# Optimization experiments

Hardware: AMD Instinct MI355X
Metric: run time of the kernel (lower is better)

The kernel has to match this reference:

```python
import jax, jax.numpy as jnp
import numpy as np

V, P, T = 30522, 1024, 2
D, H, F, L = 768, 12, 3072, 4
HD = D // H
EPS = 1e-12


def layer_norm(x, g, b):
    mu = jnp.mean(x, axis=-1, keepdims=True)
    var = jnp.mean((x - mu) ** 2, axis=-1, keepdims=True)
    return (x - mu) * jax.lax.rsqrt(var + EPS) * g + b


def setup_inputs() -> dict:
    key = jax.random.key(0)
    ks = iter(jax.random.split(key, 32))
    s = 0.02
    inp = {
        "x": jax.random.randint(next(ks), (4, 1024), 0, V, dtype=jnp.int32),
        "word_emb": jax.random.normal(next(ks), (V, D), jnp.float32) * s,
        "pos_emb": jax.random.normal(next(ks), (P, D), jnp.float32) * s,
        "type_emb": jax.random.normal(next(ks), (T, D), jnp.float32) * s,
        "emb_g": jnp.ones((D,), jnp.float32),
        "emb_b": jnp.zeros((D,), jnp.float32),
        "Wq": jax.random.normal(next(ks), (L, D, D), jnp.float32) * s,
        "bq": jnp.zeros((L, D), jnp.float32),
        "Wk": jax.random.normal(next(ks), (L, D, D), jnp.float32) * s,
        "bk": jnp.zeros((L, D), jnp.float32),
        "Wv": jax.random.normal(next(ks), (L, D, D), jnp.float32) * s,
        "bv": jnp.zeros((L, D), jnp.float32),
        "Wo": jax.random.normal(next(ks), (L, D, D), jnp.float32) * s,
        "bo": jnp.zeros((L, D), jnp.float32),
        "ln1_g": jnp.ones((L, D), jnp.float32),
        "ln1_b": jnp.zeros((L, D), jnp.float32),
        "W1": jax.random.normal(next(ks), (L, D, F), jnp.float32) * s,
        "b1": jnp.zeros((L, F), jnp.float32),
        "W2": jax.random.normal(next(ks), (L, F, D), jnp.float32) * s,
        "b2": jnp.zeros((L, D), jnp.float32),
        "ln2_g": jnp.ones((L, D), jnp.float32),
        "ln2_b": jnp.zeros((L, D), jnp.float32),
        "Wp": jax.random.normal(next(ks), (D, D), jnp.float32) * s,
        "bp": jnp.zeros((D,), jnp.float32),
    }
    return inp


def _bert_forward(x, word_emb, pos_emb, type_emb, emb_g, emb_b,
                  Wq, bq, Wk, bk, Wv, bv, Wo, bo, ln1_g, ln1_b,
                  W1, b1, W2, b2, ln2_g, ln2_b, Wp, bp):
    B, S = x.shape
    # Embeddings (token_type_ids are all zeros in the original forward)
    h = word_emb[x] + pos_emb[:S][None, :, :] + type_emb[0][None, None, :]
    h = layer_norm(h, emb_g, emb_b)

    scale = 1.0 / np.sqrt(HD).astype(np.float32)

    def step(h, p):
        (wq, bq_, wk, bk_, wv, bv_, wo, bo_, g1, b1_, w1, bi1, w2, bi2, g2, b2_) = p
        q = (h @ wq + bq_).reshape(B, S, H, HD)
        k = (h @ wk + bk_).reshape(B, S, H, HD)
        v = (h @ wv + bv_).reshape(B, S, H, HD)
        att = jnp.einsum("bqhd,bkhd->bhqk", q, k) * scale
        att = jax.nn.softmax(att, axis=-1)
        o = jnp.einsum("bhqk,bkhd->bqhd", att, v).reshape(B, S, D)
        # attention output: dense + residual + LN
        h = layer_norm(o @ wo + bo_ + h, g1, b1_)
        # FFN (note: original applies GELU twice and has NO residual here)
        inter = jax.nn.gelu(h @ w1 + bi1, approximate=False)
        h = layer_norm(jax.nn.gelu(inter @ w2 + bi2, approximate=False), g2, b2_)
        return h, None

    params = (Wq, bq, Wk, bk, Wv, bv, Wo, bo, ln1_g, ln1_b, W1, b1, W2, b2, ln2_g, ln2_b)
    h, _ = jax.lax.scan(step, h, params)
    # Pooler on final hidden states (loop in original overwrites output each iter)
    return jnp.tanh(h[:, 0] @ Wp + bp)


def reference(x, word_emb, pos_emb, type_emb, emb_g, emb_b,
              Wq, bq, Wk, bk, Wv, bv, Wo, bo, ln1_g, ln1_b,
              W1, b1, W2, b2, ln2_g, ln2_b, Wp, bp):
    return _bert_forward(x, word_emb, pos_emb, type_emb, emb_g, emb_b,
                         Wq, bq, Wk, bk, Wv, bv, Wo, bo, ln1_g, ln1_b,
                         W1, b1, W2, b2, ln2_g, ln2_b, Wp, bp)
```

## Files before the change

kernel.cpp:

```cpp
#include <hip/hip_runtime.h>
#include <math.h>

namespace {

constexpr int B  = 4;
constexpr int S  = 1024;
constexpr int D  = 768;
constexpr int H  = 12;
constexpr int HD = 64;
constexpr int F  = 3072;
constexpr int L  = 4;
constexpr int M  = B * S;
constexpr int NQKV = 3 * D;
constexpr int NQK = 2 * D;

typedef __attribute__((ext_vector_type(4))) float    f32x4;
typedef _Float16 f16x8 __attribute__((ext_vector_type(8)));
typedef __attribute__((ext_vector_type(8))) unsigned short u16x8;
typedef __attribute__((ext_vector_type(4))) unsigned short u16x4;

__device__ __forceinline__ unsigned short f2h_u(float f) {
    _Float16 h = (_Float16)f;
    return __builtin_bit_cast(unsigned short, h);
}
__device__ __forceinline__ float h2f(unsigned short u) {
    return (float)__builtin_bit_cast(_Float16, u);
}

__device__ __forceinline__ void gload16(const void* gptr, void* ldsptr) {
    __builtin_amdgcn_global_load_lds(
        (const __attribute__((address_space(1))) unsigned int*)gptr,
        (__attribute__((address_space(3))) unsigned int*)ldsptr,
        16, 0, 0);
}

__device__ __forceinline__ float wave_sum(float v) {
#pragma unroll
    for (int off = 32; off; off >>= 1) v += __shfl_xor(v, off, 64);
    return v;
}
__device__ __forceinline__ float block_sum256(float v, float* sm) {
    v = wave_sum(v);
    __syncthreads();
    if ((threadIdx.x & 63) == 0) sm[threadIdx.x >> 6] = v;
    __syncthreads();
    return sm[0] + sm[1] + sm[2] + sm[3];
}

__device__ __forceinline__ void transpose_tile(const float* __restrict__ src,
                                               unsigned short* __restrict__ dst,
                                               int R, int C) {
    __shared__ float tile[32][33];
    const int cb = blockIdx.x * 32, rb = blockIdx.y * 32;
    const int t = threadIdx.x;
    {
        const int r = t >> 3, cq = (t & 7) * 4;
        const float4 v = *(const float4*)&src[(size_t)(rb + r) * C + cb + cq];
        tile[r][cq + 0] = v.x; tile[r][cq + 1] = v.y;
        tile[r][cq + 2] = v.z; tile[r][cq + 3] = v.w;
    }
    __syncthreads();
    {
        const int dc = t >> 3, rq = (t & 7) * 4;
        u16x4 o;
#pragma unroll
        for (int j = 0; j < 4; ++j) o[j] = f2h_u(tile[rq + j][dc]);
        *(u16x4*)&dst[(size_t)(cb + dc) * R + rb + rq] = o;
    }
}

__global__ __launch_bounds__(256) void transpose_qkvo_kernel(
    const float* __restrict__ Wq, const float* __restrict__ Wk,
    const float* __restrict__ Wv, const float* __restrict__ Wo,
    unsigned short* __restrict__ Wqkv_t, unsigned short* __restrict__ Wo_t) {
    const int z = blockIdx.z;
    const int l = z >> 2, which = z & 3;
    const float* src = (which == 0 ? Wq : which == 1 ? Wk : which == 2 ? Wv : Wo)
                       + (size_t)l * D * D;
    unsigned short* dst = (which < 3)
        ? Wqkv_t + ((size_t)l * NQKV + which * D) * D
        : Wo_t + (size_t)l * D * D;
    transpose_tile(src, dst, D, D);
}

__global__ __launch_bounds__(256) void transpose_w_kernel(
    const float* __restrict__ src0, unsigned short* __restrict__ dst0, int R, int C) {
    const int l = blockIdx.z;
    transpose_tile(src0 + (size_t)l * R * C, dst0 + (size_t)l * R * C, R, C);
}

__global__ __launch_bounds__(256) void bias_concat_kernel(
    const float* __restrict__ bq, const float* __restrict__ bk,
    const float* __restrict__ bv, float* __restrict__ bqkv) {
    const int i = blockIdx.x * 256 + threadIdx.x;
    if (i >= L * NQKV) return;
    const int l = i / NQKV, j = i % NQKV;
    float v = (j < D) ? bq[l * D + j] : (j < 2 * D) ? bk[l * D + j - D] : bv[l * D + j - 2 * D];
    bqkv[i] = v;
}

__global__ __launch_bounds__(256) void embed_ln_kernel(
    const int* __restrict__ x, const float* __restrict__ we,
    const float* __restrict__ pe, const float* __restrict__ te,
    const float* __restrict__ g, const float* __restrict__ bb,
    float* __restrict__ hres, unsigned short* __restrict__ hh) {
    __shared__ float sm[4];
    const int row = blockIdx.x;
    const int s = row & (S - 1);
    const int tok = x[row];
    const int t = threadIdx.x;
    const bool act = t < 192;
    const int d = t * 4;
    float v[4] = {};
    if (act) {
        const float4 w = *(const float4*)&we[(size_t)tok * D + d];
        const float4 p = *(const float4*)&pe[(size_t)s * D + d];
        const float4 tt = *(const float4*)&te[d];
        v[0] = w.x + p.x + tt.x; v[1] = w.y + p.y + tt.y;
        v[2] = w.z + p.z + tt.z; v[3] = w.w + p.w + tt.w;
    }
    const float mu = block_sum256(v[0] + v[1] + v[2] + v[3], sm) * (1.0f / D);
    float lvar = 0.f;
    if (act) {
#pragma unroll
        for (int i = 0; i < 4; ++i) { float dv = v[i] - mu; lvar += dv * dv; }
    }
    const float var = block_sum256(lvar, sm) * (1.0f / D);
    const float inv = rsqrtf(var + 1e-12f);
    if (act) {
        const float4 g4 = *(const float4*)&g[d];
        const float4 b4 = *(const float4*)&bb[d];
        float o[4];
        o[0] = (v[0] - mu) * inv * g4.x + b4.x;
        o[1] = (v[1] - mu) * inv * g4.y + b4.y;
        o[2] = (v[2] - mu) * inv * g4.z + b4.z;
        o[3] = (v[3] - mu) * inv * g4.w + b4.w;
        *(float4*)&hres[(size_t)row * D + d] = make_float4(o[0], o[1], o[2], o[3]);
        u16x4 ob;
#pragma unroll
        for (int i = 0; i < 4; ++i) ob[i] = f2h_u(o[i]);
        *(u16x4*)&hh[(size_t)row * D + d] = ob;
    }
}

template <int NP, bool GELU_, bool HAS_RES>
__global__ __launch_bounds__(256) void ln_reduce_kernel(
    const unsigned short* __restrict__ parts,
    const float* __restrict__ bias,
    const float* __restrict__ res,
    const float* __restrict__ g, const float* __restrict__ bb,
    float* __restrict__ outres, unsigned short* __restrict__ outh) {
    __shared__ float sm[4];
    const int row = blockIdx.x;
    const int t = threadIdx.x;
    const bool act = t < 192;
    const int d = t * 4;
    float v[4] = {};
    if (act) {
        const float4 bi = *(const float4*)&bias[d];
        v[0] = bi.x; v[1] = bi.y; v[2] = bi.z; v[3] = bi.w;
#pragma unroll
        for (int pp = 0; pp < NP; ++pp) {
            const u16x4 pu = *(const u16x4*)&parts[(size_t)pp * M * D + (size_t)row * D + d];
#pragma unroll
            for (int i = 0; i < 4; ++i) v[i] += h2f(pu[i]);
        }
        if (HAS_RES) {
            const float4 rv = *(const float4*)&res[(size_t)row * D + d];
            v[0] += rv.x; v[1] += rv.y; v[2] += rv.z; v[3] += rv.w;
        }
        if (GELU_) {
#pragma unroll
            for (int i = 0; i < 4; ++i)
                v[i] = 0.5f * v[i] * (1.0f + erff(v[i] * 0.70710678118654752f));
        }
    }
    const float mu = block_sum256(v[0] + v[1] + v[2] + v[3], sm) * (1.0f / D);
    float lvar = 0.f;
    if (act) {
#pragma unroll
        for (int i = 0; i < 4; ++i) { float dv = v[i] - mu; lvar += dv * dv; }
    }
    const float var = block_sum256(lvar, sm) * (1.0f / D);
    const float inv = rsqrtf(var + 1e-12f);
    if (act) {
        const float4 g4 = *(const float4*)&g[d];
        const float4 b4 = *(const float4*)&bb[d];
        float o[4];
        o[0] = (v[0] - mu) * inv * g4.x + b4.x;
        o[1] = (v[1] - mu) * inv * g4.y + b4.y;
        o[2] = (v[2] - mu) * inv * g4.z + b4.z;
        o[3] = (v[3] - mu) * inv * g4.w + b4.w;
        *(float4*)&outres[(size_t)row * D + d] = make_float4(o[0], o[1], o[2], o[3]);
        u16x4 ob;
#pragma unroll
        for (int i = 0; i < 4; ++i) ob[i] = f2h_u(o[i]);
        *(u16x4*)&outh[(size_t)row * D + d] = ob;
    }
}

#define GEMM_STAGE(buf, k0)                                                          \
    do {                                                                             \
        gload16(Ab + (size_t)(rowBase + r0) * LDA + (k0) + c0 * 8, &Asl[buf][ldsOff0]); \
        gload16(Ab + (size_t)(rowBase + r1) * LDA + (k0) + c1 * 8, &Asl[buf][ldsOff1]); \
        gload16(Bb + (size_t)(colBase + r0) * LDA + (k0) + c0 * 8, &Bsl[buf][ldsOff0]); \
        gload16(Bb + (size_t)(colBase + r1) * LDA + (k0) + c1 * 8, &Bsl[buf][ldsOff1]); \
    } while (0)

#define GEMM_BODY(A_, Bw_, LDA_, KLEN_)                                              \
    constexpr int BK = 32;                                                           \
    __shared__ unsigned short Asl[3][128 * BK];                                      \
    __shared__ unsigned short Bsl[3][128 * BK];                                      \
    const unsigned short* Ab = (A_);                                                 \
    const unsigned short* Bb = (Bw_);                                                \
    const int LDA = (LDA_);                                                          \
    const int t = threadIdx.x;                                                       \
    const int lane = t & 63;                                                         \
    const int wid = t >> 6;                                                          \
    const int lr = lane & 15;                                                        \
    const int kh = lane >> 4;                                                        \
    const int wrBase = (wid >> 1) * 64;                                              \
    const int wcBase = (wid & 1) * 64;                                               \
    const int rowBase = blockIdx.y * 128;                                            \
    const int colBase = blockIdx.x * 128;                                            \
    f32x4 acc[4][4] = {};                                                            \
    const int r0 = t >> 2, c0 = (t & 3) ^ ((r0 >> 1) & 3);                           \
    const int s_hi = 256 + t;                                                        \
    const int r1 = s_hi >> 2, c1 = (s_hi & 3) ^ ((r1 >> 1) & 3);                     \
    const unsigned ldsOff0 = (unsigned)((t & 192) * 8);                              \
    const unsigned ldsOff1 = (unsigned)((256 + (t & 192)) * 8);                      \
    const int nt = (KLEN_) / BK;                                                     \
    GEMM_STAGE(0, 0);                                                                \
    GEMM_STAGE(1, BK);                                                               \
    int p = 0;                                                                       \
    for (int tt = 0; tt < nt; ++tt) {                                                \
        if (tt + 1 < nt) asm volatile("s_waitcnt vmcnt(4)" ::: "memory");            \
        else             asm volatile("s_waitcnt vmcnt(0)" ::: "memory");            \
        __builtin_amdgcn_s_barrier();                                                \
        __builtin_amdgcn_sched_barrier(0);                                           \
        if (tt + 2 < nt) {                                                           \
            int nb = p + 2; if (nb >= 3) nb -= 3;                                    \
            GEMM_STAGE(nb, (tt + 2) * BK);                                           \
        }                                                                            \
        f16x8 af[4], bfr[4];                                                         \
        _Pragma("unroll")                                                            \
        for (int mi = 0; mi < 4; ++mi) {                                             \
            const int ar = wrBase + mi * 16 + lr;                                    \
            const int ch = kh ^ ((ar >> 1) & 3);                                     \
            af[mi] = *(const f16x8*)&Asl[p][ar * BK + ch * 8];                       \
        }                                                                            \
        _Pragma("unroll")                                                            \
        for (int nj = 0; nj < 4; ++nj) {                                             \
            const int bc = wcBase + nj * 16 + lr;                                    \
            const int ch = kh ^ ((bc >> 1) & 3);                                     \
            bfr[nj] = *(const f16x8*)&Bsl[p][bc * BK + ch * 8];                      \
        }                                                                            \
        _Pragma("unroll")                                                            \
        for (int mi = 0; mi < 4; ++mi)                                               \
            _Pragma("unroll")                                                        \
            for (int nj = 0; nj < 4; ++nj)                                           \
                acc[mi][nj] = __builtin_amdgcn_mfma_f32_16x16x32_f16(                \
                    af[mi], bfr[nj], acc[mi][nj], 0, 0, 0);                          \
        p = (p == 2) ? 0 : p + 1;                                                    \
    }

template <int EPI, typename CT>
__global__ __launch_bounds__(256) void gemm_mfma_kernel(
    const unsigned short* __restrict__ A, const unsigned short* __restrict__ Bw,
    const float* __restrict__ bias, CT* __restrict__ C, int N, int K) {
    GEMM_BODY(A, Bw, K, K)
#pragma unroll
    for (int nj = 0; nj < 4; ++nj) {
        const int col = colBase + wcBase + nj * 16 + lr;
        const float bc = bias[col];
#pragma unroll
        for (int mi = 0; mi < 4; ++mi) {
            const int row = rowBase + wrBase + mi * 16 + kh * 4;
#pragma unroll
            for (int j = 0; j < 4; ++j) {
                float v = acc[mi][nj][j] + bc;
                if (EPI == 1) v = 0.5f * v * (1.0f + erff(v * 0.70710678118654752f));
                if constexpr (sizeof(CT) == 4) C[(size_t)(row + j) * N + col] = v;
                else                           C[(size_t)(row + j) * N + col] = f2h_u(v);
            }
        }
    }
}

__global__ __launch_bounds__(256) void gemm_splitk_kernel(
    const unsigned short* __restrict__ A, const unsigned short* __restrict__ Bw,
    unsigned short* __restrict__ Cpart, int N, int Kfull, int Kc) {
    const int z = blockIdx.z;
    GEMM_BODY(A + (size_t)z * Kc, Bw + (size_t)z * Kc, Kfull, Kc)
    unsigned short* Cp = Cpart + (size_t)z * M * N;
#pragma unroll
    for (int nj = 0; nj < 4; ++nj) {
        const int col = colBase + wcBase + nj * 16 + lr;
#pragma unroll
        for (int mi = 0; mi < 4; ++mi) {
            const int row = rowBase + wrBase + mi * 16 + kh * 4;
#pragma unroll
            for (int j = 0; j < 4; ++j)
                Cp[(size_t)(row + j) * N + col] = f2h_u(acc[mi][nj][j]);
        }
    }
}

__global__ __launch_bounds__(256) void gemm_qkv_kernel(
    const unsigned short* __restrict__ A, const unsigned short* __restrict__ Bw,
    const float* __restrict__ bias, unsigned short* __restrict__ qkout,
    unsigned short* __restrict__ vtout) {
    GEMM_BODY(A, Bw, D, D)
    const bool isV = (colBase >= NQK);
#pragma unroll
    for (int nj = 0; nj < 4; ++nj) {
        const int col = colBase + wcBase + nj * 16 + lr;
        const float bc = bias[col];
        if (!isV) {
#pragma unroll
            for (int mi = 0; mi < 4; ++mi) {
                const int row = rowBase + wrBase + mi * 16 + kh * 4;
#pragma unroll
                for (int j = 0; j < 4; ++j)
                    qkout[(size_t)(row + j) * NQK + col] = f2h_u(acc[mi][nj][j] + bc);
            }
        } else {
            const int dd = col - NQK;
            const int h2 = dd >> 6, d6 = dd & 63;
#pragma unroll
            for (int mi = 0; mi < 4; ++mi) {
                const int row = rowBase + wrBase + mi * 16 + kh * 4;
                const int b2 = row >> 10, s2 = row & 1023;
                u16x4 ov;
#pragma unroll
                for (int j = 0; j < 4; ++j) ov[j] = f2h_u(acc[mi][nj][j] + bc);
                *(u16x4*)&vtout[(((size_t)(b2 * H + h2)) * 64 + d6) * S + s2] = ov;
            }
        }
    }
}

__global__ __launch_bounds__(256) void attention_kernel(
    const unsigned short* __restrict__ qk,
    const unsigned short* __restrict__ vt,
    unsigned short* __restrict__ o) {
    __shared__ unsigned short Qs[64 * 64];
    __shared__ unsigned short Ks[2][64 * 64];
    __shared__ unsigned short Vt[2][64 * 64];
    __shared__ _Float16 Ps[4][16 * 64];

    const int t = threadIdx.x;
    const int qt = blockIdx.x;
    const int bh = blockIdx.y;
    const int b = bh / H, hh = bh % H;
    const int w = t >> 6;
    const int lr = t & 15;
    const int kh = (t >> 4) & 3;

    const int r0 = t >> 3;
    const int g0 = (t & 7) ^ (r0 & 7);
    const unsigned lo0 = (unsigned)((t & 192) * 8);
    const unsigned lo1 = (unsigned)(2048 + (t & 192) * 8);

    const unsigned short* kgb = qk + D + hh * HD;
    const unsigned short* vgb = vt + (size_t)bh * 64 * S;

    {
        const size_t qrow0 = (size_t)(b * S + qt * 64);
        gload16(qk + (qrow0 + r0) * NQK + hh * HD + g0 * 8, &Qs[lo0]);
        gload16(qk + (qrow0 + r0 + 32) * NQK + hh * HD + g0 * 8, &Qs[lo1]);
        gload16(kgb + (size_t)(b * S + r0) * NQK + g0 * 8, &Ks[0][lo0]);
        gload16(kgb + (size_t)(b * S + r0 + 32) * NQK + g0 * 8, &Ks[0][lo1]);
        gload16(vgb + (size_t)r0 * S + g0 * 8, &Vt[0][lo0]);
        gload16(vgb + (size_t)(r0 + 32) * S + g0 * 8, &Vt[0][lo1]);
    }
    __syncthreads();

    float m_[4] = {-INFINITY, -INFINITY, -INFINITY, -INFINITY};
    float l_[4] = {};
    f32x4 oacc[4] = {};
    const int swlo = (kh)     ^ (lr & 7);
    const int swhi = (kh + 4) ^ (lr & 7);
    constexpr int NT = S / 64;

    for (int it = 0; it < NT; ++it) {
        const int cur = it & 1;
        if (it + 1 < NT) {
            const int kt = (it + 1) * 64;
            gload16(kgb + (size_t)(b * S + kt + r0) * NQK + g0 * 8, &Ks[cur ^ 1][lo0]);
            gload16(kgb + (size_t)(b * S + kt + r0 + 32) * NQK + g0 * 8, &Ks[cur ^ 1][lo1]);
            gload16(vgb + (size_t)r0 * S + kt + g0 * 8, &Vt[cur ^ 1][lo0]);
            gload16(vgb + (size_t)(r0 + 32) * S + kt + g0 * 8, &Vt[cur ^ 1][lo1]);
        }

        const int qr = w * 16 + lr;
        f16x8 aq0 = *(const f16x8*)&Qs[qr * 64 + swlo * 8];
        f16x8 aq1 = *(const f16x8*)&Qs[qr * 64 + swhi * 8];
        f32x4 sc[4];
        __builtin_amdgcn_s_setprio(1);
#pragma unroll
        for (int nj = 0; nj < 4; ++nj) {
            const int kr = nj * 16 + lr;
            f16x8 b0 = *(const f16x8*)&Ks[cur][kr * 64 + swlo * 8];
            f16x8 b1 = *(const f16x8*)&Ks[cur][kr * 64 + swhi * 8];
            f32x4 z = {};
            z = __builtin_amdgcn_mfma_f32_16x16x32_f16(aq0, b0, z, 0, 0, 0);
            z = __builtin_amdgcn_mfma_f32_16x16x32_f16(aq1, b1, z, 0, 0, 0);
            sc[nj] = z;
        }
        __builtin_amdgcn_s_setprio(0);

        float alpha[4];
#pragma unroll
        for (int j = 0; j < 4; ++j) {
            float rm = fmaxf(fmaxf(sc[0][j], sc[1][j]), fmaxf(sc[2][j], sc[3][j])) * 0.125f;
#pragma unroll
            for (int off = 1; off < 16; off <<= 1) rm = fmaxf(rm, __shfl_xor(rm, off, 64));
            const float mn = fmaxf(m_[j], rm);
            alpha[j] = __expf(m_[j] - mn);
            m_[j] = mn;
        }
        float ph[4][4];
        float rs[4] = {};
#pragma unroll
        for (int nj = 0; nj < 4; ++nj)
#pragma unroll
            for (int j = 0; j < 4; ++j) {
                float p2 = __expf(fmaf(sc[nj][j], 0.125f, -m_[j]));
                ph[nj][j] = p2;
                rs[j] += p2;
            }
#pragma unroll
        for (int j = 0; j < 4; ++j) {
#pragma unroll
            for (int off = 1; off < 16; off <<= 1) rs[j] += __shfl_xor(rs[j], off, 64);
            l_[j] = l_[j] * alpha[j] + rs[j];
        }
        _Float16* psw = &Ps[w][0];
#pragma unroll
        for (int nj = 0; nj < 4; ++nj)
#pragma unroll
            for (int j = 0; j < 4; ++j) {
                const int pr = kh * 4 + j;
                const int pc = nj * 16 + lr;
                psw[pr * 64 + (((pc >> 3) ^ (pr & 7)) * 8) + (pc & 7)] = (_Float16)ph[nj][j];
            }
#pragma unroll
        for (int nj = 0; nj < 4; ++nj)
#pragma unroll
            for (int j = 0; j < 4; ++j) oacc[nj][j] *= alpha[j];

        f16x8 pa0 = *(const f16x8*)&psw[lr * 64 + swlo * 8];
        f16x8 pa1 = *(const f16x8*)&psw[lr * 64 + swhi * 8];
        __builtin_amdgcn_s_setprio(1);
#pragma unroll
        for (int nj = 0; nj < 4; ++nj) {
            const int vr = nj * 16 + lr;
            f16x8 b0 = *(const f16x8*)&Vt[cur][vr * 64 + swlo * 8];
            f16x8 b1 = *(const f16x8*)&Vt[cur][vr * 64 + swhi * 8];
            oacc[nj] = __builtin_amdgcn_mfma_f32_16x16x32_f16(pa0, b0, oacc[nj], 0, 0, 0);
            oacc[nj] = __builtin_amdgcn_mfma_f32_16x16x32_f16(pa1, b1, oacc[nj], 0, 0, 0);
        }
        __builtin_amdgcn_s_setprio(0);

        __syncthreads();
    }

    float inv[4];
#pragma unroll
    for (int j = 0; j < 4; ++j) inv[j] = 1.0f / l_[j];
#pragma unroll
    for (int nj = 0; nj < 4; ++nj)
#pragma unroll
        for (int j = 0; j < 4; ++j) {
            const int token = b * S + qt * 64 + w * 16 + kh * 4 + j;
            o[(size_t)token * D + hh * HD + nj * 16 + lr] = f2h_u(oacc[nj][j] * inv[j]);
        }
}

__global__ __launch_bounds__(768) void pooler_partial_kernel(
    const float* __restrict__ h, const float* __restrict__ Wp,
    float* __restrict__ partial) {
    const int slice = blockIdx.x;
    const int b = blockIdx.y;
    const int d = threadIdx.x;
    const float* hrow = h + (size_t)b * S * D + slice * 48;
    const float* wcol = Wp + (size_t)slice * 48 * D + d;
    float acc = 0.f;
#pragma unroll
    for (int kk = 0; kk < 48; ++kk) acc = fmaf(hrow[kk], wcol[(size_t)kk * D], acc);
    partial[((size_t)b * 16 + slice) * D + d] = acc;
}

__global__ __launch_bounds__(768) void pooler_reduce_kernel(
    const float* __restrict__ partial, const float* __restrict__ bp,
    float* __restrict__ out) {
    const int b = blockIdx.x;
    const int d = threadIdx.x;
    float acc = bp[d];
#pragma unroll
    for (int s2 = 0; s2 < 16; ++s2) acc += partial[((size_t)b * 16 + s2) * D + d];
    out[(size_t)b * D + d] = tanhf(acc);
}

}

extern "C" void kernel_launch(void* const* d_in, const int* in_sizes, int n_in,
                              void* d_out, int out_size, void* d_ws, size_t ws_size,
                              hipStream_t stream) {
    (void)in_sizes; (void)n_in; (void)out_size; (void)ws_size;

    const int*   x     = (const int*)  d_in[0];
    const float* we    = (const float*)d_in[1];
    const float* pe    = (const float*)d_in[2];
    const float* te    = (const float*)d_in[3];
    const float* emb_g = (const float*)d_in[4];
    const float* emb_b = (const float*)d_in[5];
    const float* Wq    = (const float*)d_in[6];
    const float* bq    = (const float*)d_in[7];
    const float* Wk    = (const float*)d_in[8];
    const float* bk    = (const float*)d_in[9];
    const float* Wv    = (const float*)d_in[10];
    const float* bv    = (const float*)d_in[11];
    const float* Wo    = (const float*)d_in[12];
    const float* bo    = (const float*)d_in[13];
    const float* ln1_g = (const float*)d_in[14];
    const float* ln1_b = (const float*)d_in[15];
    const float* W1    = (const float*)d_in[16];
    const float* b1    = (const float*)d_in[17];
    const float* W2    = (const float*)d_in[18];
    const float* b2    = (const float*)d_in[19];
    const float* ln2_g = (const float*)d_in[20];
    const float* ln2_b = (const float*)d_in[21];
    const float* Wp    = (const float*)d_in[22];
    const float* bp    = (const float*)d_in[23];

    char* wp8 = (char*)d_ws;
    float*          h_res  = (float*)wp8;              wp8 += (size_t)M * D * 4;
    unsigned short* h_f16  = (unsigned short*)wp8;     wp8 += (size_t)M * D * 2;
    unsigned short* blockA = (unsigned short*)wp8;     wp8 += (size_t)M * F * 2;
    unsigned short* qk_f   = blockA;
    unsigned short* v_t    = blockA + (size_t)M * NQK;
    unsigned short* attno  = v_t + (size_t)B * H * 64 * S;
    unsigned short* inter  = blockA;
    unsigned short* wo_part = blockA;
    char*           oproj8 = wp8;                      wp8 += (size_t)M * D * 4;
    unsigned short* f2_part = (unsigned short*)oproj8;
    unsigned short* Wqkv_t = (unsigned short*)wp8;     wp8 += (size_t)L * NQKV * D * 2;
    unsigned short* Wo_t   = (unsigned short*)wp8;     wp8 += (size_t)L * D * D * 2;
    unsigned short* W1_t   = (unsigned short*)wp8;     wp8 += (size_t)L * F * D * 2;
    unsigned short* W2_t   = (unsigned short*)wp8;     wp8 += (size_t)L * D * F * 2;
    float*          bqkv   = (float*)wp8;              wp8 += (size_t)L * NQKV * 4;
    float*          ppart  = (float*)wp8;

    transpose_qkvo_kernel<<<dim3(24, 24, 16), 256, 0, stream>>>(Wq, Wk, Wv, Wo, Wqkv_t, Wo_t);
    transpose_w_kernel<<<dim3(96, 24, 4), 256, 0, stream>>>(W1, W1_t, D, F);
    transpose_w_kernel<<<dim3(24, 96, 4), 256, 0, stream>>>(W2, W2_t, F, D);
    bias_concat_kernel<<<dim3((L * NQKV + 255) / 256), 256, 0, stream>>>(bq, bk, bv, bqkv);

    embed_ln_kernel<<<M, 256, 0, stream>>>(x, we, pe, te, emb_g, emb_b, h_res, h_f16);

    for (int l = 0; l < L; ++l) {
        gemm_qkv_kernel<<<dim3(NQKV / 128, M / 128), 256, 0, stream>>>(
            h_f16, Wqkv_t + (size_t)l * NQKV * D, bqkv + l * NQKV, qk_f, v_t);

        attention_kernel<<<dim3(S / 64, B * H), 256, 0, stream>>>(qk_f, v_t, attno);

        gemm_splitk_kernel<<<dim3(D / 128, M / 128, 3), 256, 0, stream>>>(
            attno, Wo_t + (size_t)l * D * D, wo_part, D, D, 256);
        ln_reduce_kernel<3, false, true><<<M, 256, 0, stream>>>(
            wo_part, bo + l * D, h_res, ln1_g + l * D, ln1_b + l * D, h_res, h_f16);

        gemm_mfma_kernel<1, unsigned short><<<dim3(F / 128, M / 128), 256, 0, stream>>>(
            h_f16, W1_t + (size_t)l * F * D, b1 + l * F, inter, F, D);

        gemm_splitk_kernel<<<dim3(D / 128, M / 128, 2), 256, 0, stream>>>(
            inter, W2_t + (size_t)l * D * F, f2_part, D, F, 1536);
        ln_reduce_kernel<2, true, false><<<M, 256, 0, stream>>>(
            f2_part, b2 + l * D, nullptr, ln2_g + l * D, ln2_b + l * D, h_res, h_f16);
    }

    pooler_partial_kernel<<<dim3(16, B), 768, 0, stream>>>(h_res, Wp, ppart);
    pooler_reduce_kernel<<<B, 768, 0, stream>>>(ppart, bp, (float*)d_out);
}
```

Baseline: 773.4 us.

## Swizzle workgroups across XCDs, raise MFMA priority, split W2 GEMM three ways

Workgroup IDs in the GEMM body and the attention kernel are remapped so that consecutive tiles are spread across the eight XCDs in groups, aiming for better L2 locality of shared A/B tiles. The attention launch becomes a flat 1D grid to support this mapping. The MFMA block is wrapped in s_setprio raise/lower so waves issuing matrix math get scheduling priority. The W2 GEMM moves from a 2-way to a 3-way split-K, with the third partial written into the now-idle h_f16 buffer, and ln_reduce gains a second partial source to sum it. This adds more parallel blocks and an extra partial read, in exchange for more reduction traffic.

Result: faster. 720.5 us, median of 2 (-6.8%).

```diff
diff --git a/kernel.cpp b/kernel.cpp
--- a/kernel.cpp
+++ b/kernel.cpp
@@ -143,9 +143,10 @@
     }
 }
 
-template <int NP, bool GELU_, bool HAS_RES>
+template <int NPA, int NPB, bool GELU_, bool HAS_RES>
 __global__ __launch_bounds__(256) void ln_reduce_kernel(
-    const unsigned short* __restrict__ parts,
+    const unsigned short* __restrict__ pA,
+    const unsigned short* __restrict__ pB,
     const float* __restrict__ bias,
     const float* __restrict__ res,
     const float* __restrict__ g, const float* __restrict__ bb,
@@ -160,8 +161,14 @@
         const float4 bi = *(const float4*)&bias[d];
         v[0] = bi.x; v[1] = bi.y; v[2] = bi.z; v[3] = bi.w;
 #pragma unroll
-        for (int pp = 0; pp < NP; ++pp) {
-            const u16x4 pu = *(const u16x4*)&parts[(size_t)pp * M * D + (size_t)row * D + d];
+        for (int pp = 0; pp < NPA; ++pp) {
+            const u16x4 pu = *(const u16x4*)&pA[(size_t)pp * M * D + (size_t)row * D + d];
+#pragma unroll
+            for (int i = 0; i < 4; ++i) v[i] += h2f(pu[i]);
+        }
+#pragma unroll
+        for (int pp = 0; pp < NPB; ++pp) {
+            const u16x4 pu = *(const u16x4*)&pB[(size_t)pp * M * D + (size_t)row * D + d];
 #pragma unroll
             for (int i = 0; i < 4; ++i) v[i] += h2f(pu[i]);
         }
@@ -221,8 +228,11 @@
     const int kh = lane >> 4;                                                        \
     const int wrBase = (wid >> 1) * 64;                                              \
     const int wcBase = (wid & 1) * 64;                                               \
-    const int rowBase = blockIdx.y * 128;                                            \
-    const int colBase = blockIdx.x * 128;                                            \
+    const int nwg = gridDim.x * gridDim.y;                                           \
+    const int flatid = blockIdx.y * gridDim.x + blockIdx.x;                          \
+    const int swzid = (flatid & 7) * (nwg >> 3) + (flatid >> 3);                     \
+    const int rowBase = (swzid / gridDim.x) * 128;                                   \
+    const int colBase = (swzid % gridDim.x) * 128;                                   \
     f32x4 acc[4][4] = {};                                                            \
     const int r0 = t >> 2, c0 = (t & 3) ^ ((r0 >> 1) & 3);                           \
     const int s_hi = 256 + t;                                                        \
@@ -255,12 +265,14 @@
             const int ch = kh ^ ((bc >> 1) & 3);                                     \
             bfr[nj] = *(const f16x8*)&Bsl[p][bc * BK + ch * 8];                      \
         }                                                                            \
+        __builtin_amdgcn_s_setprio(1);                                               \
         _Pragma("unroll")                                                            \
         for (int mi = 0; mi < 4; ++mi)                                               \
             _Pragma("unroll")                                                        \
             for (int nj = 0; nj < 4; ++nj)                                           \
                 acc[mi][nj] = __builtin_amdgcn_mfma_f32_16x16x32_f16(                \
                     af[mi], bfr[nj], acc[mi][nj], 0, 0, 0);                          \
+        __builtin_amdgcn_s_setprio(0);                                               \
         p = (p == 2) ? 0 : p + 1;                                                    \
     }
 
@@ -289,10 +301,12 @@
 
 __global__ __launch_bounds__(256) void gemm_splitk_kernel(
     const unsigned short* __restrict__ A, const unsigned short* __restrict__ Bw,
-    unsigned short* __restrict__ Cpart, int N, int Kfull, int Kc) {
+    unsigned short* __restrict__ CpA, unsigned short* __restrict__ CpB,
+    int ZA, int N, int Kfull, int Kc) {
     const int z = blockIdx.z;
     GEMM_BODY(A + (size_t)z * Kc, Bw + (size_t)z * Kc, Kfull, Kc)
-    unsigned short* Cp = Cpart + (size_t)z * M * N;
+    unsigned short* Cp = (z < ZA) ? (CpA + (size_t)z * M * N)
+                                  : (CpB + (size_t)(z - ZA) * M * N);
 #pragma unroll
     for (int nj = 0; nj < 4; ++nj) {
         const int col = colBase + wcBase + nj * 16 + lr;
@@ -350,8 +364,11 @@
     __shared__ _Float16 Ps[4][16 * 64];
 
     const int t = threadIdx.x;
-    const int qt = blockIdx.x;
-    const int bh = blockIdx.y;
+    const int nwg = gridDim.x;
+    const int flatid = blockIdx.x;
+    const int lin = (flatid & 7) * (nwg >> 3) + (flatid >> 3);
+    const int qt = lin & 15;
+    const int bh = lin >> 4;
     const int b = bh / H, hh = bh % H;
     const int w = t >> 6;
     const int lr = t & 15;
@@ -564,20 +581,20 @@
         gemm_qkv_kernel<<<dim3(NQKV / 128, M / 128), 256, 0, stream>>>(
             h_f16, Wqkv_t + (size_t)l * NQKV * D, bqkv + l * NQKV, qk_f, v_t);
 
-        attention_kernel<<<dim3(S / 64, B * H), 256, 0, stream>>>(qk_f, v_t, attno);
+        attention_kernel<<<(S / 64) * B * H, 256, 0, stream>>>(qk_f, v_t, attno);
 
         gemm_splitk_kernel<<<dim3(D / 128, M / 128, 3), 256, 0, stream>>>(
-            attno, Wo_t + (size_t)l * D * D, wo_part, D, D, 256);
-        ln_reduce_kernel<3, false, true><<<M, 256, 0, stream>>>(
-            wo_part, bo + l * D, h_res, ln1_g + l * D, ln1_b + l * D, h_res, h_f16);
+            attno, Wo_t + (size_t)l * D * D, wo_part, nullptr, 3, D, D, 256);
+        ln_reduce_kernel<3, 0, false, true><<<M, 256, 0, stream>>>(
+            wo_part, nullptr, bo + l * D, h_res, ln1_g + l * D, ln1_b + l * D, h_res, h_f16);
 
         gemm_mfma_kernel<1, unsigned short><<<dim3(F / 128, M / 128), 256, 0, stream>>>(
             h_f16, W1_t + (size_t)l * F * D, b1 + l * F, inter, F, D);
 
-        gemm_splitk_kernel<<<dim3(D / 128, M / 128, 2), 256, 0, stream>>>(
-            inter, W2_t + (size_t)l * D * F, f2_part, D, F, 1536);
-        ln_reduce_kernel<2, true, false><<<M, 256, 0, stream>>>(
-            f2_part, b2 + l * D, nullptr, ln2_g + l * D, ln2_b + l * D, h_res, h_f16);
+        gemm_splitk_kernel<<<dim3(D / 128, M / 128, 3), 256, 0, stream>>>(
+            inter, W2_t + (size_t)l * D * F, f2_part, h_f16, 2, D, F, 1024);
+        ln_reduce_kernel<2, 1, true, false><<<M, 256, 0, stream>>>(
+            f2_part, h_f16, b2 + l * D, nullptr, ln2_g + l * D, ln2_b + l * D, h_res, h_f16);
     }
 
     pooler_partial_kernel<<<dim3(16, B), 768, 0, stream>>>(h_res, Wp, ppart);
```
